# Performance work log

Measured on AMD Instinct MI355X. Metric: run time of the kernel, lower is better.

## Reference

```python
import jax, jax.numpy as jnp
import numpy as np
from jax.ops import segment_sum, segment_max

N, E, F_IN, H, C, NCLS = 50000, 800000, 128, 2, 64, 16
NEG_SLOPE = 0.2


def setup_inputs() -> dict:
    key = jax.random.key(0)
    ks = jax.random.split(key, 10)
    x = jax.random.normal(ks[0], (N, F_IN), dtype=jnp.float32)
    edge_index = jax.random.randint(ks[1], (2, E), 0, N, dtype=jnp.int32)
    edge_attr = jax.random.uniform(ks[2], (E,), dtype=jnp.float32)
    W1 = jax.random.normal(ks[3], (F_IN, H * C), dtype=jnp.float32) / np.sqrt(F_IN).astype(np.float32)
    att_src1 = jax.random.normal(ks[4], (H, C), dtype=jnp.float32) * 0.1
    att_dst1 = jax.random.normal(ks[5], (H, C), dtype=jnp.float32) * 0.1
    b1 = jnp.zeros((H * C,), dtype=jnp.float32)
    W2 = jax.random.normal(ks[6], (H * C, NCLS), dtype=jnp.float32) / np.sqrt(H * C).astype(np.float32)
    att_src2 = jax.random.normal(ks[7], (1, NCLS), dtype=jnp.float32) * 0.1
    att_dst2 = jax.random.normal(ks[8], (1, NCLS), dtype=jnp.float32) * 0.1
    b2 = jnp.zeros((NCLS,), dtype=jnp.float32)
    return {"x": x, "edge_index": edge_index, "edge_attr": edge_attr,
            "W1": W1, "att_src1": att_src1, "att_dst1": att_dst1, "b1": b1,
            "W2": W2, "att_src2": att_src2, "att_dst2": att_dst2, "b2": b2}


def gat_conv(x, src, dst, W, a_src, a_dst, b):
    # x: [N,Fin]; W: [Fin,H*C]; a_src/a_dst: [H,C]
    n = x.shape[0]
    h_heads, c = a_src.shape
    h = (x @ W).reshape(n, h_heads, c)                       # [N,H,C]
    alpha_src = jnp.einsum('nhc,hc->nh', h, a_src)           # [N,H]
    alpha_dst = jnp.einsum('nhc,hc->nh', h, a_dst)           # [N,H]
    e = jax.nn.leaky_relu(alpha_src[src] + alpha_dst[dst], NEG_SLOPE)  # [Etot,H]
    # segment softmax over incoming edges of each dst node (self-loops guarantee non-empty segments)
    e_max = segment_max(e, dst, num_segments=n)              # [N,H]
    p = jnp.exp(e - e_max[dst])
    denom = segment_sum(p, dst, num_segments=n)              # [N,H]
    alpha = p / (denom[dst] + 1e-16)                         # [Etot,H]
    out = segment_sum(h[src] * alpha[:, :, None], dst, num_segments=n)  # [N,H,C]
    return out.reshape(n, h_heads * c) + b


def reference(x, edge_index, edge_attr, W1, att_src1, att_dst1, b1, W2, att_src2, att_dst2, b2):
    # edge_attr is accepted but unused: GATConv has edge_dim=None so edge features are ignored.
    # Dropout layers (p=0.6) are inactive in eval mode.
    n = x.shape[0]
    loop = jnp.arange(n, dtype=edge_index.dtype)             # self-loops (PyG add_self_loops=True)
    src = jnp.concatenate([edge_index[0], loop])
    dst = jnp.concatenate([edge_index[1], loop])
    h = jax.nn.elu(gat_conv(x, src, dst, W1, att_src1, att_dst1, b1))
    out = gat_conv(h, src, dst, W2, att_src2, att_dst2, b2)
    return jax.nn.log_softmax(out, axis=1)
```

## Files before the change

kernel.cpp:

```cpp
#include <hip/hip_runtime.h>
#include <math.h>

#define FIN   128
#define HC1   128
#define NCLS  16
#define NEG_SLOPE 0.2f

typedef __attribute__((ext_vector_type(8))) short bf16x8;
typedef __attribute__((ext_vector_type(4))) float f32x4;
typedef __attribute__((ext_vector_type(2))) float f32x2;

__device__ __forceinline__ unsigned short f2bf_rne(float f) {
    unsigned int u = __float_as_uint(f);
    unsigned int r = u + 0x7FFFu + ((u >> 16) & 1u);
    return (unsigned short)(r >> 16);
}
__device__ __forceinline__ float bf2f(unsigned short h) {
    return __uint_as_float(((unsigned int)h) << 16);
}

__device__ __forceinline__ unsigned char f2fp8(float v) {
    int p = __builtin_amdgcn_cvt_pk_fp8_f32(v, v, 0, false);
    return (unsigned char)(p & 0xFF);
}

#define EPB 4096

__device__ __forceinline__
void gemm1_body(const float* __restrict__ x, const float* __restrict__ W,
                const float* __restrict__ a_src, const float* __restrict__ a_dst,
                unsigned char* __restrict__ h1q, float* __restrict__ as1,
                float* __restrict__ ad1, int N, int bid, float4* smem) {
    unsigned short* whi = (unsigned short*)smem;
    unsigned short* wlo = whi + FIN * HC1;
    int tid = threadIdx.x;

#pragma unroll
    for (int i = 0; i < 64; ++i) {
        int idx = tid + i * 256;
        int k = idx >> 7, c = idx & 127;
        float v = W[idx];
        unsigned short hb = f2bf_rne(v);
        unsigned short lb = f2bf_rne(v - bf2f(hb));
        int kb = k >> 5, kk = k & 31;
        int g = kk >> 3, j = kk & 7;
        int ct = c >> 4, li = c & 15;
        int off = ((kb * 8 + ct) * 64 + g * 16 + li) * 8 + j;
        whi[off] = hb;
        wlo[off] = lb;
    }

    int wid = tid >> 6, lane = tid & 63;
    int li = lane & 15, g = lane >> 4;
    int rowbase = bid * 64 + wid * 16;

    int arow = rowbase + li;
    if (arow >= N) arow = N - 1;
    const float* xp = x + (long)arow * FIN + g * 8;
    bf16x8 Ahi[4], Alo[4];
#pragma unroll
    for (int kb = 0; kb < 4; ++kb) {
        float4 v0 = *reinterpret_cast<const float4*>(xp + kb * 32);
        float4 v1 = *reinterpret_cast<const float4*>(xp + kb * 32 + 4);
        float vs0 = v0.x, vs1 = v0.y, vs2 = v0.z, vs3 = v0.w;
        float vs4 = v1.x, vs5 = v1.y, vs6 = v1.z, vs7 = v1.w;
        bf16x8 h8, l8;
        unsigned short hb;
        hb = f2bf_rne(vs0); h8[0] = (short)hb; l8[0] = (short)f2bf_rne(vs0 - bf2f(hb));
        hb = f2bf_rne(vs1); h8[1] = (short)hb; l8[1] = (short)f2bf_rne(vs1 - bf2f(hb));
        hb = f2bf_rne(vs2); h8[2] = (short)hb; l8[2] = (short)f2bf_rne(vs2 - bf2f(hb));
        hb = f2bf_rne(vs3); h8[3] = (short)hb; l8[3] = (short)f2bf_rne(vs3 - bf2f(hb));
        hb = f2bf_rne(vs4); h8[4] = (short)hb; l8[4] = (short)f2bf_rne(vs4 - bf2f(hb));
        hb = f2bf_rne(vs5); h8[5] = (short)hb; l8[5] = (short)f2bf_rne(vs5 - bf2f(hb));
        hb = f2bf_rne(vs6); h8[6] = (short)hb; l8[6] = (short)f2bf_rne(vs6 - bf2f(hb));
        hb = f2bf_rne(vs7); h8[7] = (short)hb; l8[7] = (short)f2bf_rne(vs7 - bf2f(hb));
        Ahi[kb] = h8; Alo[kb] = l8;
    }

    float asr[8], adr[8];
#pragma unroll
    for (int ct = 0; ct < 8; ++ct) {
        asr[ct] = a_src[ct * 16 + li];
        adr[ct] = a_dst[ct * 16 + li];
    }

    __syncthreads();

    f32x4 acc[8];
#pragma unroll
    for (int ct = 0; ct < 8; ++ct) acc[ct] = (f32x4){0.f, 0.f, 0.f, 0.f};

#pragma unroll
    for (int kb = 0; kb < 4; ++kb) {
#pragma unroll
        for (int ct = 0; ct < 8; ++ct) {
            bf16x8 bh = *reinterpret_cast<const bf16x8*>(&whi[((kb * 8 + ct) * 64 + lane) * 8]);
            bf16x8 bl = *reinterpret_cast<const bf16x8*>(&wlo[((kb * 8 + ct) * 64 + lane) * 8]);
            acc[ct] = __builtin_amdgcn_mfma_f32_16x16x32_bf16(Alo[kb], bh, acc[ct], 0, 0, 0);
            acc[ct] = __builtin_amdgcn_mfma_f32_16x16x32_bf16(Ahi[kb], bl, acc[ct], 0, 0, 0);
            acc[ct] = __builtin_amdgcn_mfma_f32_16x16x32_bf16(Ahi[kb], bh, acc[ct], 0, 0, 0);
        }
    }

#pragma unroll
    for (int q = 0; q < 4; ++q) {
        int n = rowbase + g * 4 + q;
        bool valid = (n < N);
        float p0s = 0.f, p1s = 0.f, p0d = 0.f, p1d = 0.f;
#pragma unroll
        for (int ct = 0; ct < 8; ++ct) {
            float h = acc[ct][q];
            if (valid) h1q[(long)n * HC1 + ct * 16 + li] = f2fp8(h);
            if (ct < 4) { p0s = fmaf(h, asr[ct], p0s); p0d = fmaf(h, adr[ct], p0d); }
            else        { p1s = fmaf(h, asr[ct], p1s); p1d = fmaf(h, adr[ct], p1d); }
        }
#pragma unroll
        for (int off = 8; off >= 1; off >>= 1) {
            p0s += __shfl_xor(p0s, off, 16);
            p1s += __shfl_xor(p1s, off, 16);
            p0d += __shfl_xor(p0d, off, 16);
            p1d += __shfl_xor(p1d, off, 16);
        }
        if (valid && li == 0) {
            as1[n * 2 + 0] = p0s; as1[n * 2 + 1] = p1s;
            ad1[n * 2 + 0] = p0d; ad1[n * 2 + 1] = p1d;
        }
    }
}

__global__ __launch_bounds__(256)
void f_bcnt(const int* __restrict__ ei, int* __restrict__ blockhist, int E, int NB,
            const float* __restrict__ x, const float* __restrict__ W1,
            const float* __restrict__ a_src, const float* __restrict__ a_dst,
            unsigned char* __restrict__ h1q, float* __restrict__ as1,
            float* __restrict__ ad1, int N, int nb_csr, int gemm_base) {
    __shared__ float4 smem[4096];
    int tid = threadIdx.x;
    if ((int)blockIdx.x >= nb_csr) {
        gemm1_body(x, W1, a_src, a_dst, h1q, as1, ad1, N,
                   gemm_base + blockIdx.x - nb_csr, smem);
        return;
    }
    int* h = (int*)smem;
    h[tid] = 0;
    __syncthreads();
    int base = blockIdx.x * EPB;
#pragma unroll
    for (int j = 0; j < EPB / 256; ++j) {
        int e = base + j * 256 + tid;
        if (e < E) atomicAdd(&h[ei[E + e] >> 8], 1);
    }
    __syncthreads();
    if (tid < NB) blockhist[blockIdx.x * NB + tid] = h[tid];
}

__global__ __launch_bounds__(256)
void f_colscan(int* __restrict__ blockhist, int* __restrict__ colsum, int EB, int NB,
               const float* __restrict__ x, const float* __restrict__ W1,
               const float* __restrict__ a_src, const float* __restrict__ a_dst,
               unsigned char* __restrict__ h1q, float* __restrict__ as1,
               float* __restrict__ ad1, int N, int nb_csr, int gemm_base) {
    __shared__ float4 smem[4096];
    int b = threadIdx.x;
    if ((int)blockIdx.x >= nb_csr) {
        gemm1_body(x, W1, a_src, a_dst, h1q, as1, ad1, N,
                   gemm_base + blockIdx.x - nb_csr, smem);
        return;
    }
    int* lds = (int*)smem;
    int t = blockIdx.x;
    int v = (b < EB) ? blockhist[b * NB + t] : 0;
    lds[b] = v;
    __syncthreads();
    for (int off = 1; off < 256; off <<= 1) {
        int u = (b >= off) ? lds[b - off] : 0;
        __syncthreads();
        lds[b] += u;
        __syncthreads();
    }
    if (b < EB) blockhist[b * NB + t] = lds[b] - v;
    if (b == 255) colsum[t] = lds[255];
}

__global__ __launch_bounds__(256)
void bscan2_kernel(const int* __restrict__ colsum, int* __restrict__ bucket_base,
                   int NB, const float* __restrict__ W2,
                   const float* __restrict__ a_src2, const float* __restrict__ a_dst2,
                   float* __restrict__ w2T, float* __restrict__ w2s,
                   float* __restrict__ w2d) {
    __shared__ int lds[256];
    int t = threadIdx.x;
    int v = (t < NB) ? colsum[t] : 0;
    lds[t] = v;
    __syncthreads();
    for (int off = 1; off < 256; off <<= 1) {
        int u = (t >= off) ? lds[t - off] : 0;
        __syncthreads();
        lds[t] += u;
        __syncthreads();
    }
    if (t < NB) bucket_base[t] = lds[t] - v;
    if (t == 255) bucket_base[NB] = lds[255];

    if (t < FIN) {
        float s = 0.f, d = 0.f;
#pragma unroll
        for (int c = 0; c < NCLS; ++c) {
            float w = W2[t * NCLS + c];
            w2T[c * FIN + t] = w;
            s = fmaf(w, a_src2[c], s);
            d = fmaf(w, a_dst2[c], d);
        }
        w2s[t] = s; w2d[t] = d;
    }
}

__global__ __launch_bounds__(256)
void f_binA(const int* __restrict__ ei, const int* __restrict__ blockhist,
            const int* __restrict__ bucket_base, int* __restrict__ tmp,
            int E, int NB,
            const float* __restrict__ x, const float* __restrict__ W1,
            const float* __restrict__ a_src, const float* __restrict__ a_dst,
            unsigned char* __restrict__ h1q, float* __restrict__ as1,
            float* __restrict__ ad1, int N, int nb_csr, int gemm_base) {
    __shared__ float4 smem[4096];
    int tid = threadIdx.x;
    if ((int)blockIdx.x >= nb_csr) {
        gemm1_body(x, W1, a_src, a_dst, h1q, as1, ad1, N,
                   gemm_base + blockIdx.x - nb_csr, smem);
        return;
    }
    int* h  = (int*)smem;
    int* bb = h + 256;
    h[tid] = 0;
    if (tid < NB) bb[tid] = blockhist[blockIdx.x * NB + tid] + bucket_base[tid];
    __syncthreads();
    int base = blockIdx.x * EPB;
#pragma unroll
    for (int j = 0; j < EPB / 256; ++j) {
        int e = base + j * 256 + tid;
        if (e < E) {
            int s = ei[e], d = ei[E + e];
            int b = d >> 8;
            int r = atomicAdd(&h[b], 1);
            tmp[bb[b] + r] = (s << 8) | (d & 255);
        }
    }
}

__global__ __launch_bounds__(256)
void f_binB(const int* __restrict__ tmp, const int* __restrict__ bucket_base,
            int* __restrict__ csr, int* __restrict__ eoffs, int E, int N,
            const float* __restrict__ x, const float* __restrict__ W1,
            const float* __restrict__ a_src, const float* __restrict__ a_dst,
            unsigned char* __restrict__ h1q, float* __restrict__ as1,
            float* __restrict__ ad1, int nb_csr, int gemm_base) {
    __shared__ float4 smem[4096];
    int t = threadIdx.x;
    if ((int)blockIdx.x >= nb_csr) {
        gemm1_body(x, W1, a_src, a_dst, h1q, as1, ad1, N,
                   gemm_base + blockIdx.x - nb_csr, smem);
        return;
    }
    int* cnt = (int*)smem;
    int* lds = cnt + 256;
    int* cur = cnt + 512;
    int b = blockIdx.x;
    int lo = bucket_base[b], hi = bucket_base[b + 1];
    cnt[t] = 0;
    __syncthreads();
    for (int i = lo + t; i < hi; i += 256)
        atomicAdd(&cnt[tmp[i] & 255], 1);
    __syncthreads();
    int v = cnt[t];
    lds[t] = v;
    __syncthreads();
    for (int off = 1; off < 256; off <<= 1) {
        int u = (t >= off) ? lds[t - off] : 0;
        __syncthreads();
        lds[t] += u;
        __syncthreads();
    }
    int excl = lds[t] - v;
    int node = b * 256 + t;
    if (node < N) eoffs[node] = lo + excl;
    if (b == 0 && t == 0) eoffs[N] = E;
    cur[t] = lo + excl;
    __syncthreads();
    for (int i = lo + t; i < hi; i += 256) {
        int e = tmp[i];
        int p = atomicAdd(&cur[e & 255], 1);
        csr[p] = ((unsigned int)e) >> 8;
    }
}

__global__ __launch_bounds__(256)
void fgather1(const int* __restrict__ eoffs, const int* __restrict__ csr,
              const float* __restrict__ as_arr, const float* __restrict__ ad_arr,
              const unsigned char* __restrict__ h1q, const float* __restrict__ b1,
              const float* __restrict__ w2T, const float* __restrict__ w2s,
              const float* __restrict__ w2d,
              float* __restrict__ zout, float* __restrict__ as2,
              float* __restrict__ ad2, int N) {
    int tid = threadIdx.x;
    int g = tid >> 5;
    int l = tid & 31;
    int n = blockIdx.x * 8 + g;
    if (n >= N) return;
    int head = l >> 4;
    int s0 = eoffs[n], s1 = eoffs[n + 1];

    float ad0 = ad_arr[2 * n], ad1v = ad_arr[2 * n + 1];
    float2 aself = *reinterpret_cast<const float2*>(&as_arr[2 * n]);
    float vs0 = aself.x + ad0;  vs0 = (vs0 >= 0.f) ? vs0 : NEG_SLOPE * vs0;
    float vs1 = aself.y + ad1v; vs1 = (vs1 >= 0.f) ? vs1 : NEG_SLOPE * vs1;
    float adn = head ? ad1v : ad0;

    float ps = __expf(head ? vs1 : vs0);
    unsigned int us = *reinterpret_cast<const unsigned int*>(&h1q[((long)n << 7) + 4 * l]);
    f32x2 slo = __builtin_amdgcn_cvt_pk_f32_fp8(us, false);
    f32x2 shi = __builtin_amdgcn_cvt_pk_f32_fp8(us, true);
    float4 acc;
    acc.x = slo[0] * ps; acc.y = slo[1] * ps;
    acc.z = shi[0] * ps; acc.w = shi[1] * ps;
    float den = ps;

    int i = s0;
    for (; i + 8 <= s1; i += 8) {
        int se[8];
#pragma unroll
        for (int j = 0; j < 8; ++j) se[j] = csr[i + j];
        float av[8];
#pragma unroll
        for (int j = 0; j < 8; ++j) av[j] = as_arr[2 * se[j] + head];
        unsigned int u[8];
#pragma unroll
        for (int j = 0; j < 8; ++j)
            u[j] = *reinterpret_cast<const unsigned int*>(&h1q[((long)se[j] << 7) + 4 * l]);
        float w[8];
#pragma unroll
        for (int j = 0; j < 8; ++j) {
            float v = av[j] + adn; v = (v >= 0.f) ? v : NEG_SLOPE * v;
            w[j] = __expf(v);
            den += w[j];
        }
#pragma unroll
        for (int j = 0; j < 8; ++j) {
            f32x2 lo = __builtin_amdgcn_cvt_pk_f32_fp8(u[j], false);
            f32x2 hi = __builtin_amdgcn_cvt_pk_f32_fp8(u[j], true);
            acc.x = fmaf(lo[0], w[j], acc.x);
            acc.y = fmaf(lo[1], w[j], acc.y);
            acc.z = fmaf(hi[0], w[j], acc.z);
            acc.w = fmaf(hi[1], w[j], acc.w);
        }
    }
    for (; i < s1; ++i) {
        int s = csr[i];
        float av = as_arr[2 * s + head];
        unsigned int u = *reinterpret_cast<const unsigned int*>(&h1q[((long)s << 7) + 4 * l]);
        float v = av + adn; v = (v >= 0.f) ? v : NEG_SLOPE * v;
        float w = __expf(v);
        den += w;
        f32x2 lo = __builtin_amdgcn_cvt_pk_f32_fp8(u, false);
        f32x2 hi = __builtin_amdgcn_cvt_pk_f32_fp8(u, true);
        acc.x = fmaf(lo[0], w, acc.x);
        acc.y = fmaf(lo[1], w, acc.y);
        acc.z = fmaf(hi[0], w, acc.z);
        acc.w = fmaf(hi[1], w, acc.w);
    }
    float r = 1.f / (den + 1e-16f);
    int col = 4 * l;
    float4 bb = *reinterpret_cast<const float4*>(&b1[col]);
    float4 o;
    o.x = acc.x * r + bb.x; o.y = acc.y * r + bb.y;
    o.z = acc.z * r + bb.z; o.w = acc.w * r + bb.w;
    o.x = (o.x > 0.f) ? o.x : expm1f(o.x);
    o.y = (o.y > 0.f) ? o.y : expm1f(o.y);
    o.z = (o.z > 0.f) ? o.z : expm1f(o.z);
    o.w = (o.w > 0.f) ? o.w : expm1f(o.w);

    float4 ws4 = *reinterpret_cast<const float4*>(&w2s[col]);
    float4 wd4 = *reinterpret_cast<const float4*>(&w2d[col]);
    float sa2 = o.x * ws4.x + o.y * ws4.y + o.z * ws4.z + o.w * ws4.w;
    float da2 = o.x * wd4.x + o.y * wd4.y + o.z * wd4.z + o.w * wd4.w;
#pragma unroll
    for (int off = 16; off >= 1; off >>= 1) {
        sa2 += __shfl_xor(sa2, off, 32);
        da2 += __shfl_xor(da2, off, 32);
    }
    if (l == 0) { as2[n] = sa2; ad2[n] = da2; }

    float zp[NCLS];
#pragma unroll
    for (int c = 0; c < NCLS; ++c) {
        float4 w4 = *reinterpret_cast<const float4*>(&w2T[c * FIN + col]);
        zp[c] = o.x * w4.x + o.y * w4.y + o.z * w4.z + o.w * w4.w;
    }
    int bsel = (l >> 4) & 1;
    float z8[8];
#pragma unroll
    for (int j = 0; j < 8; ++j) {
        float send = bsel ? zp[j] : zp[j + 8];
        float keep = bsel ? zp[j + 8] : zp[j];
        z8[j] = keep + __shfl_xor(send, 16, 32);
    }
    bsel = (l >> 3) & 1;
    float z4v[4];
#pragma unroll
    for (int j = 0; j < 4; ++j) {
        float send = bsel ? z8[j] : z8[j + 4];
        float keep = bsel ? z8[j + 4] : z8[j];
        z4v[j] = keep + __shfl_xor(send, 8, 32);
    }
    bsel = (l >> 2) & 1;
    float z2v[2];
#pragma unroll
    for (int j = 0; j < 2; ++j) {
        float send = bsel ? z4v[j] : z4v[j + 2];
        float keep = bsel ? z4v[j + 2] : z4v[j];
        z2v[j] = keep + __shfl_xor(send, 4, 32);
    }
    bsel = (l >> 1) & 1;
    float z1v;
    {
        float send = bsel ? z2v[0] : z2v[1];
        float keep = bsel ? z2v[1] : z2v[0];
        z1v = keep + __shfl_xor(send, 2, 32);
    }
    z1v += __shfl_xor(z1v, 1, 32);
    if (!(l & 1)) zout[(long)n * NCLS + ((l >> 1) & 15)] = z1v;
}

__global__ __launch_bounds__(256)
void fgather2(const int* __restrict__ eoffs, const int* __restrict__ csr,
              const float* __restrict__ as2, const float* __restrict__ ad2,
              const float* __restrict__ z, const float* __restrict__ b2,
              float* __restrict__ out, int N) {
    int g = threadIdx.x >> 4;
    int l = threadIdx.x & 15;
    int n = blockIdx.x * 16 + g;
    if (n >= N) return;
    int s0 = eoffs[n], s1 = eoffs[n + 1];
    float adn = ad2[n];
    float vs = as2[n] + adn; vs = (vs >= 0.f) ? vs : NEG_SLOPE * vs;

    float ps = __expf(vs);
    float acc = ps * z[(long)n * NCLS + l];
    float den = ps;
    int i = s0;
    for (; i + 4 <= s1; i += 4) {
        int sa = csr[i], sb = csr[i + 1], sc = csr[i + 2], sd = csr[i + 3];
        float aa = as2[sa], ab = as2[sb], ac = as2[sc], ad = as2[sd];
        float za = z[sa * NCLS + l];
        float zb = z[sb * NCLS + l];
        float zc = z[sc * NCLS + l];
        float zd = z[sd * NCLS + l];
        float va = aa + adn; va = (va >= 0.f) ? va : NEG_SLOPE * va;
        float vb = ab + adn; vb = (vb >= 0.f) ? vb : NEG_SLOPE * vb;
        float vc = ac + adn; vc = (vc >= 0.f) ? vc : NEG_SLOPE * vc;
        float vd = ad + adn; vd = (vd >= 0.f) ? vd : NEG_SLOPE * vd;
        float pa = __expf(va);
        float pb = __expf(vb);
        float pc = __expf(vc);
        float pd = __expf(vd);
        den += pa + pb + pc + pd;
        acc = fmaf(za, pa, acc);
        acc = fmaf(zb, pb, acc);
        acc = fmaf(zc, pc, acc);
        acc = fmaf(zd, pd, acc);
    }
    for (; i < s1; ++i) {
        int s = csr[i];
        float v = as2[s] + adn; v = (v >= 0.f) ? v : NEG_SLOPE * v;
        float p = __expf(v);
        den += p;
        acc = fmaf(z[s * NCLS + l], p, acc);
    }

    float o = acc / (den + 1e-16f) + b2[l];

    float mx = o;
#pragma unroll
    for (int off = 8; off >= 1; off >>= 1) mx = fmaxf(mx, __shfl_xor(mx, off, 16));
    float ex = __expf(o - mx);
    float sum = ex;
#pragma unroll
    for (int off = 8; off >= 1; off >>= 1) sum += __shfl_xor(sum, off, 16);
    out[(long)n * NCLS + l] = o - mx - __logf(sum);
}

extern "C" void kernel_launch(void* const* d_in, const int* in_sizes, int n_in,
                              void* d_out, int out_size, void* d_ws, size_t ws_size,
                              hipStream_t stream) {
    const float* x        = (const float*)d_in[0];
    const int*   ei       = (const int*)  d_in[1];
    const float* W1       = (const float*)d_in[3];
    const float* att_src1 = (const float*)d_in[4];
    const float* att_dst1 = (const float*)d_in[5];
    const float* b1       = (const float*)d_in[6];
    const float* W2       = (const float*)d_in[7];
    const float* att_src2 = (const float*)d_in[8];
    const float* att_dst2 = (const float*)d_in[9];
    const float* b2       = (const float*)d_in[10];
    float* out = (float*)d_out;

    const int N = in_sizes[0] / FIN;
    const int E = in_sizes[1] / 2;
    const int NB = (N + 255) >> 8;
    const int EB = (E + EPB - 1) / EPB;
    const int GB = (N + 63) / 64;

    int q = GB / 4, rr = GB % 4;
    int g0 = q + (rr > 0 ? 1 : 0);
    int g1 = q + (rr > 1 ? 1 : 0);
    int g2 = q + (rr > 2 ? 1 : 0);
    int g3 = q;
    int b0 = 0, b1o = g0, b2o = g0 + g1, b3o = g0 + g1 + g2;

    char* ws = (char*)d_ws;
    size_t off = 0;
    auto alloc = [&](size_t bytes) { char* p = ws + off; off += (bytes + 255) & ~(size_t)255; return p; };
    int*    blockhist     = (int*)  alloc((size_t)EB * NB * 4);
    int*    colsum        = (int*)  alloc((size_t)NB * 4);
    int*    bucket_base   = (int*)  alloc((size_t)(NB + 1) * 4);
    int*    tmp           = (int*)  alloc((size_t)E * 4);
    int*    csr           = (int*)  alloc((size_t)E * 4);
    int*    eoffs         = (int*)  alloc((size_t)(N + 1) * 4);
    unsigned char* h1q    = (unsigned char*)alloc((size_t)N * HC1);
    float*  z             = (float*) alloc((size_t)N * NCLS * 4);
    float*  as1           = (float*) alloc((size_t)N * 2 * 4);
    float*  ad1           = (float*) alloc((size_t)N * 2 * 4);
    float*  as2           = (float*) alloc((size_t)N * 4);
    float*  ad2           = (float*) alloc((size_t)N * 4);
    float*  w2T           = (float*) alloc((size_t)NCLS * FIN * 4);
    float*  w2s           = (float*) alloc((size_t)FIN * 4);
    float*  w2d           = (float*) alloc((size_t)FIN * 4);
    (void)ws_size;

    f_bcnt<<<EB + g0, 256, 0, stream>>>(ei, blockhist, E, NB,
        x, W1, att_src1, att_dst1, h1q, as1, ad1, N, EB, b0);
    f_colscan<<<NB + g1, 256, 0, stream>>>(blockhist, colsum, EB, NB,
        x, W1, att_src1, att_dst1, h1q, as1, ad1, N, NB, b1o);
    bscan2_kernel<<<1, 256, 0, stream>>>(colsum, bucket_base, NB,
                                         W2, att_src2, att_dst2, w2T, w2s, w2d);
    f_binA<<<EB + g2, 256, 0, stream>>>(ei, blockhist, bucket_base, tmp, E, NB,
        x, W1, att_src1, att_dst1, h1q, as1, ad1, N, EB, b2o);
    f_binB<<<NB + g3, 256, 0, stream>>>(tmp, bucket_base, csr, eoffs, E, N,
        x, W1, att_src1, att_dst1, h1q, as1, ad1, NB, b3o);

    fgather1<<<(N + 7) / 8, 256, 0, stream>>>(
        eoffs, csr, as1, ad1, h1q, b1, w2T, w2s, w2d, z, as2, ad2, N);
    fgather2<<<(N + 15) / 16, 256, 0, stream>>>(eoffs, csr, as2, ad2, z, b2, out, N);
}
```

Before: 101.8 us.

## Compute layer-1 edge weights cooperatively per chunk and stage them in LDS

The layer-1 gather previously had every lane redundantly load the source index and attention score and compute exp for each edge. Now the 16 lanes of each head split a 64-edge chunk, compute the weights once, and store them with the source indices in shared memory. The accumulation loop then reads them from LDS, and the denominator comes from a 16-lane shuffle reduction. There is no barrier between the LDS writes and reads within the 32-lane group, which relies on lockstep execution inside a wavefront. The change also adds LDS traffic and a serial chunk loop in exchange for fewer exp and global loads.

Result: faster. 96.29 us (-5.4%).

```diff
diff --git a/kernel.cpp b/kernel.cpp
--- a/kernel.cpp
+++ b/kernel.cpp
@@ -294,6 +294,8 @@
     }
 }
 
+#define CH 64
+
 __global__ __launch_bounds__(256)
 void fgather1(const int* __restrict__ eoffs, const int* __restrict__ csr,
               const float* __restrict__ as_arr, const float* __restrict__ ad_arr,
@@ -302,12 +304,15 @@
               const float* __restrict__ w2d,
               float* __restrict__ zout, float* __restrict__ as2,
               float* __restrict__ ad2, int N) {
+    __shared__ float wbuf[8][2][CH];
+    __shared__ int   sbuf[8][CH];
     int tid = threadIdx.x;
     int g = tid >> 5;
     int l = tid & 31;
     int n = blockIdx.x * 8 + g;
     if (n >= N) return;
     int head = l >> 4;
+    int hl = l & 15;
     int s0 = eoffs[n], s1 = eoffs[n + 1];
 
     float ad0 = ad_arr[2 * n], ad1v = ad_arr[2 * n + 1];
@@ -323,51 +328,63 @@
     float4 acc;
     acc.x = slo[0] * ps; acc.y = slo[1] * ps;
     acc.z = shi[0] * ps; acc.w = shi[1] * ps;
-    float den = ps;
-
-    int i = s0;
-    for (; i + 8 <= s1; i += 8) {
-        int se[8];
-#pragma unroll
-        for (int j = 0; j < 8; ++j) se[j] = csr[i + j];
-        float av[8];
-#pragma unroll
-        for (int j = 0; j < 8; ++j) av[j] = as_arr[2 * se[j] + head];
-        unsigned int u[8];
-#pragma unroll
-        for (int j = 0; j < 8; ++j)
-            u[j] = *reinterpret_cast<const unsigned int*>(&h1q[((long)se[j] << 7) + 4 * l]);
-        float w[8];
-#pragma unroll
-        for (int j = 0; j < 8; ++j) {
-            float v = av[j] + adn; v = (v >= 0.f) ? v : NEG_SLOPE * v;
-            w[j] = __expf(v);
-            den += w[j];
-        }
-#pragma unroll
-        for (int j = 0; j < 8; ++j) {
-            f32x2 lo = __builtin_amdgcn_cvt_pk_f32_fp8(u[j], false);
-            f32x2 hi = __builtin_amdgcn_cvt_pk_f32_fp8(u[j], true);
-            acc.x = fmaf(lo[0], w[j], acc.x);
-            acc.y = fmaf(lo[1], w[j], acc.y);
-            acc.z = fmaf(hi[0], w[j], acc.z);
-            acc.w = fmaf(hi[1], w[j], acc.w);
-        }
-    }
-    for (; i < s1; ++i) {
-        int s = csr[i];
-        float av = as_arr[2 * s + head];
-        unsigned int u = *reinterpret_cast<const unsigned int*>(&h1q[((long)s << 7) + 4 * l]);
-        float v = av + adn; v = (v >= 0.f) ? v : NEG_SLOPE * v;
-        float w = __expf(v);
-        den += w;
-        f32x2 lo = __builtin_amdgcn_cvt_pk_f32_fp8(u, false);
-        f32x2 hi = __builtin_amdgcn_cvt_pk_f32_fp8(u, true);
-        acc.x = fmaf(lo[0], w, acc.x);
-        acc.y = fmaf(lo[1], w, acc.y);
-        acc.z = fmaf(hi[0], w, acc.z);
-        acc.w = fmaf(hi[1], w, acc.w);
-    }
+    float denp = 0.f;
+
+    for (int base = s0; base < s1; base += CH) {
+        int cnt = min(CH, s1 - base);
+        for (int j = hl; j < cnt; j += 16) {
+            int s = csr[base + j];
+            if (head == 0) sbuf[g][j] = s;
+            float av = as_arr[2 * s + head];
+            float v = av + adn; v = (v >= 0.f) ? v : NEG_SLOPE * v;
+            float w = __expf(v);
+            wbuf[g][head][j] = w;
+            denp += w;
+        }
+        int j = 0;
+        for (; j + 4 <= cnt; j += 4) {
+            int sa = sbuf[g][j],     sb = sbuf[g][j + 1];
+            int sc = sbuf[g][j + 2], sd = sbuf[g][j + 3];
+            float wa = wbuf[g][head][j],     wb = wbuf[g][head][j + 1];
+            float wc = wbuf[g][head][j + 2], wd = wbuf[g][head][j + 3];
+            unsigned int ua = *reinterpret_cast<const unsigned int*>(&h1q[((long)sa << 7) + 4 * l]);
+            unsigned int ub = *reinterpret_cast<const unsigned int*>(&h1q[((long)sb << 7) + 4 * l]);
+            unsigned int uc = *reinterpret_cast<const unsigned int*>(&h1q[((long)sc << 7) + 4 * l]);
+            unsigned int ud = *reinterpret_cast<const unsigned int*>(&h1q[((long)sd << 7) + 4 * l]);
+            f32x2 lo, hi;
+            lo = __builtin_amdgcn_cvt_pk_f32_fp8(ua, false);
+            hi = __builtin_amdgcn_cvt_pk_f32_fp8(ua, true);
+            acc.x = fmaf(lo[0], wa, acc.x); acc.y = fmaf(lo[1], wa, acc.y);
+            acc.z = fmaf(hi[0], wa, acc.z); acc.w = fmaf(hi[1], wa, acc.w);
+            lo = __builtin_amdgcn_cvt_pk_f32_fp8(ub, false);
+            hi = __builtin_amdgcn_cvt_pk_f32_fp8(ub, true);
+            acc.x = fmaf(lo[0], wb, acc.x); acc.y = fmaf(lo[1], wb, acc.y);
+            acc.z = fmaf(hi[0], wb, acc.z); acc.w = fmaf(hi[1], wb, acc.w);
+            lo = __builtin_amdgcn_cvt_pk_f32_fp8(uc, false);
+            hi = __builtin_amdgcn_cvt_pk_f32_fp8(uc, true);
+            acc.x = fmaf(lo[0], wc, acc.x); acc.y = fmaf(lo[1], wc, acc.y);
+            acc.z = fmaf(hi[0], wc, acc.z); acc.w = fmaf(hi[1], wc, acc.w);
+            lo = __builtin_amdgcn_cvt_pk_f32_fp8(ud, false);
+            hi = __builtin_amdgcn_cvt_pk_f32_fp8(ud, true);
+            acc.x = fmaf(lo[0], wd, acc.x); acc.y = fmaf(lo[1], wd, acc.y);
+            acc.z = fmaf(hi[0], wd, acc.z); acc.w = fmaf(hi[1], wd, acc.w);
+        }
+        for (; j < cnt; ++j) {
+            int s = sbuf[g][j];
+            float w = wbuf[g][head][j];
+            unsigned int u = *reinterpret_cast<const unsigned int*>(&h1q[((long)s << 7) + 4 * l]);
+            f32x2 lo = __builtin_amdgcn_cvt_pk_f32_fp8(u, false);
+            f32x2 hi = __builtin_amdgcn_cvt_pk_f32_fp8(u, true);
+            acc.x = fmaf(lo[0], w, acc.x); acc.y = fmaf(lo[1], w, acc.y);
+            acc.z = fmaf(hi[0], w, acc.z); acc.w = fmaf(hi[1], w, acc.w);
+        }
+    }
+
+    float den = denp;
+#pragma unroll
+    for (int off = 8; off >= 1; off >>= 1) den += __shfl_xor(den, off, 16);
+    den += ps;
+
     float r = 1.f / (den + 1e-16f);
     int col = 4 * l;
     float4 bb = *reinterpret_cast<const float4*>(&b1[col]);
```
